# Optimization experiments

Hardware: AMD Instinct MI355X
Metric: run time of the kernel (lower is better)

## Reference

```python
import jax, jax.numpy as jnp
import numpy as np

EMBED_DIM = 1024
NUM_HEADS = 16
HEAD_DIM = EMBED_DIM // NUM_HEADS
SCALE = HEAD_DIM ** -0.5


def setup_inputs() -> dict:
    key = jax.random.key(0)
    ks = jax.random.split(key, 5)
    B, N, C = 4, 2048, EMBED_DIM
    s = C ** -0.5
    return {
        "x": jax.random.normal(ks[0], (B, N, C), dtype=jnp.float32),
        "w_qkv": jax.random.normal(ks[1], (C, 3 * C), dtype=jnp.float32) * s,
        "b_qkv": jnp.zeros((3 * C,), dtype=jnp.float32),
        "w_proj": jax.random.normal(ks[2], (C, C), dtype=jnp.float32) * s,
        "b_proj": jnp.zeros((C,), dtype=jnp.float32),
    }


def reference(x, w_qkv, b_qkv, w_proj, b_proj):
    B, N, C = x.shape
    H, D = NUM_HEADS, HEAD_DIM
    qkv = x @ w_qkv + b_qkv                      # (B, N, 3C)
    qkv = qkv.reshape(B, N, 3, H, D)
    qkv = jnp.transpose(qkv, (2, 0, 3, 1, 4))    # (3, B, H, N, D)
    q, k, v = qkv[0], qkv[1], qkv[2]
    attn = jnp.einsum('bhnd,bhmd->bhnm', q, k) * SCALE
    attn = jax.nn.softmax(attn, axis=-1)
    out = jnp.einsum('bhnm,bhmd->bhnd', attn, v)  # (B, H, N, D)
    out = jnp.transpose(out, (0, 2, 1, 3)).reshape(B, N, C)
    return out @ w_proj + b_proj
```

## Files before the change

kernel.cpp:

```cpp
#include <hip/hip_runtime.h>

typedef __attribute__((ext_vector_type(8))) short short8v;
typedef __attribute__((ext_vector_type(4))) short short4v;
typedef __attribute__((ext_vector_type(4))) float float4v;
typedef __attribute__((ext_vector_type(4))) unsigned short ushort4v;
typedef __attribute__((ext_vector_type(8))) unsigned short ushort8v;

#define GLOBAL_AS __attribute__((address_space(1)))
#define LDS_AS __attribute__((address_space(3)))

__device__ __forceinline__ void async_cp16(const void* g, void* l) {
  __builtin_amdgcn_global_load_lds((const GLOBAL_AS void*)g, (LDS_AS void*)l, 16, 0, 0);
}

__device__ __forceinline__ unsigned short f2bf(float f) {
  unsigned u = __float_as_uint(f);
  u += 0x7fffu + ((u >> 16) & 1u);
  return (unsigned short)(u >> 16);
}

#if defined(__HIP_DEVICE_COMPILE__)
#if __has_builtin(__builtin_amdgcn_mfma_f32_16x16x16bf16_1k)
#define MFMA_PV(a, b, c) __builtin_amdgcn_mfma_f32_16x16x16bf16_1k(a, b, c, 0, 0, 0)
#elif __has_builtin(__builtin_amdgcn_mfma_f32_16x16x16_bf16_1k)
#define MFMA_PV(a, b, c) __builtin_amdgcn_mfma_f32_16x16x16_bf16_1k(a, b, c, 0, 0, 0)
#elif __has_builtin(__builtin_amdgcn_mfma_f32_16x16x16_bf16)
#define MFMA_PV(a, b, c) __builtin_amdgcn_mfma_f32_16x16x16_bf16(a, b, c, 0, 0, 0)
#else
#error "no 16x16x16 bf16 mfma builtin on device"
#endif
#if __has_builtin(__builtin_amdgcn_exp2f)
#define EXP2F(x) __builtin_amdgcn_exp2f(x)
#else
#define EXP2F(x) exp2f(x)
#endif
#else
#define MFMA_PV(a, b, c) (c)
#define EXP2F(x) exp2f(x)
#endif

#if defined(__HIP_DEVICE_COMPILE__) && __has_builtin(__builtin_amdgcn_cvt_pk_bf16_f32)
typedef __attribute__((ext_vector_type(2))) __bf16 bf16x2v;
__device__ __forceinline__ unsigned pk_bf16(float a, float b) {
  bf16x2v r = __builtin_amdgcn_cvt_pk_bf16_f32(a, b);
  return __builtin_bit_cast(unsigned, r);
}
#else
__device__ __forceinline__ unsigned pk_bf16(float a, float b) {
  return (unsigned)f2bf(a) | ((unsigned)f2bf(b) << 16);
}
#endif

#define MFMA_QK(a, b, c) __builtin_amdgcn_mfma_f32_16x16x32_bf16(a, b, c, 0, 0, 0)


__global__ __launch_bounds__(256) void cvt_f32_bf16(const float* __restrict__ src,
                                                    unsigned short* __restrict__ dst) {
  int i = blockIdx.x * 256 + threadIdx.x;
  float4 v = ((const float4*)src)[i];
  ushort4v o;
  o.x = f2bf(v.x); o.y = f2bf(v.y); o.z = f2bf(v.z); o.w = f2bf(v.w);
  ((ushort4v*)dst)[i] = o;
}

__global__ __launch_bounds__(256) void transpose_w(const float* __restrict__ src,
                                                   unsigned short* __restrict__ dst,
                                                   int K, int N) {
  __shared__ float tile[64][65];
  int k0 = blockIdx.x * 64, n0 = blockIdx.y * 64;
  int t = threadIdx.x;
  int tc = t & 15, tr = t >> 4;
#pragma unroll
  for (int p = 0; p < 4; p++) {
    int r = tr + p * 16;
    float4 v = *(const float4*)(src + (size_t)(k0 + r) * N + n0 + tc * 4);
    tile[r][tc * 4 + 0] = v.x; tile[r][tc * 4 + 1] = v.y;
    tile[r][tc * 4 + 2] = v.z; tile[r][tc * 4 + 3] = v.w;
  }
  __syncthreads();
#pragma unroll
  for (int p = 0; p < 4; p++) {
    int rn = tr + p * 16;
    ushort4v o;
    o.x = f2bf(tile[tc * 4 + 0][rn]);
    o.y = f2bf(tile[tc * 4 + 1][rn]);
    o.z = f2bf(tile[tc * 4 + 2][rn]);
    o.w = f2bf(tile[tc * 4 + 3][rn]);
    *(ushort4v*)(dst + (size_t)(n0 + rn) * K + k0 + tc * 4) = o;
  }
}


__global__ __launch_bounds__(256) void gemm_qkv(const unsigned short* __restrict__ A,
                                                const unsigned short* __restrict__ BT,
                                                const float* __restrict__ bias,
                                                unsigned short* __restrict__ Qo,
                                                unsigned short* __restrict__ Ko,
                                                unsigned short* __restrict__ VTo) {
  __shared__ unsigned short As[128 * 32];
  __shared__ unsigned short Bs[128 * 32];
  int tid = threadIdx.x;
  int lane = tid & 63, w = tid >> 6, g = lane >> 4, c = lane & 15;
  int m0 = blockIdx.x * 128, n0 = blockIdx.y * 128;
  int wm = (w & 1) * 64, wn = (w >> 1) * 64;
  float4v acc[4][4] = {};

  for (int k0 = 0; k0 < 1024; k0 += 32) {
    __syncthreads();
#pragma unroll
    for (int p = 0; p < 2; p++) {
      int idx = p * 256 + tid;
      int row = idx >> 2, c8 = (idx & 3) * 8;
      async_cp16(A + (size_t)(m0 + row) * 1024 + k0 + c8, &As[idx * 8]);
      async_cp16(BT + (size_t)(n0 + row) * 1024 + k0 + c8, &Bs[idx * 8]);
    }
    __syncthreads();
    short8v af[4], bf[4];
#pragma unroll
    for (int i = 0; i < 4; i++)
      af[i] = *(const short8v*)(&As[(wm + i * 16 + c) * 32 + g * 8]);
#pragma unroll
    for (int j = 0; j < 4; j++)
      bf[j] = *(const short8v*)(&Bs[(wn + j * 16 + c) * 32 + g * 8]);
#pragma unroll
    for (int i = 0; i < 4; i++)
#pragma unroll
      for (int j = 0; j < 4; j++)
        acc[i][j] = MFMA_QK(af[i], bf[j], acc[i][j]);
  }

  int which = n0 >> 10;
#pragma unroll
  for (int j = 0; j < 4; j++) {
    int ng = n0 + wn + j * 16 + c;
    float bv = bias[ng];
    int h = (ng & 1023) >> 6, d = ng & 63;
#pragma unroll
    for (int i = 0; i < 4; i++) {
#pragma unroll
      for (int r = 0; r < 4; r++) {
        int mg = m0 + wm + i * 16 + g * 4 + r;
        int b = mg >> 11, n = mg & 2047;
        float v = acc[i][j][r] + bv;
        if (which == 0)
          Qo[((size_t)(b * 16 + h) * 2048 + n) * 64 + d] = f2bf(v * 0.18033688011112042f);
        else if (which == 1)
          Ko[((size_t)(b * 16 + h) * 2048 + n) * 64 + d] = f2bf(v);
        else
          VTo[((size_t)(b * 16 + h) * 64 + d) * 2048 + n] = f2bf(v);
      }
    }
  }
}


#define NTOK 2048
#define VTS 132

__global__ __launch_bounds__(256) void attn_kernel(const unsigned short* __restrict__ Qg,
                                                   const unsigned short* __restrict__ Kg,
                                                   const unsigned short* __restrict__ VTg,
                                                   unsigned short* __restrict__ Og) {
  __shared__ unsigned short Ks[128 * 64];
  __shared__ unsigned short VTsm[64 * VTS];

  int tid = threadIdx.x;
  int lane = tid & 63, w = tid >> 6, g = lane >> 4, c = lane & 15;
  int bh = blockIdx.y;
  int q0 = blockIdx.x * 128;

  const unsigned short* Qb = Qg + (size_t)bh * NTOK * 64;
  const unsigned short* Kb = Kg + (size_t)bh * NTOK * 64;
  const unsigned short* VTb = VTg + (size_t)bh * 64 * NTOK;

  short8v qf[2][2];
#pragma unroll
  for (int nt = 0; nt < 2; nt++)
#pragma unroll
    for (int kk = 0; kk < 2; kk++)
      qf[nt][kk] = *(const short8v*)(Qb + (size_t)(q0 + w * 32 + nt * 16 + c) * 64 +
                                     kk * 32 + g * 8);

  float4v L4[2] = {};
  float4v o[2][4] = {};

  for (int kt = 0; kt < NTOK; kt += 128) {
    __syncthreads();
#pragma unroll
    for (int p = 0; p < 4; p++) {
      int idx = p * 256 + tid;
      int row = idx >> 3, ch = idx & 7;
      async_cp16(Kb + (size_t)(kt + row) * 64 + ((ch ^ (row & 7)) * 8), &Ks[idx * 8]);
    }
    ushort8v vv[4];
    int vds[4], vcs[4];
#pragma unroll
    for (int p = 0; p < 4; p++) {
      int idx = p * 256 + tid;
      int d = idx >> 4, c8 = (idx & 15) * 8;
      vv[p] = *(const ushort8v*)(VTb + (size_t)d * NTOK + kt + c8);
      vds[p] = d; vcs[p] = c8;
    }
#pragma unroll
    for (int p = 0; p < 4; p++) {
      ushort4v lo = __builtin_shufflevector(vv[p], vv[p], 0, 1, 2, 3);
      ushort4v hi = __builtin_shufflevector(vv[p], vv[p], 4, 5, 6, 7);
      *(ushort4v*)(&VTsm[vds[p] * VTS + vcs[p]]) = lo;
      *(ushort4v*)(&VTsm[vds[p] * VTS + vcs[p] + 4]) = hi;
    }
    __syncthreads();

    float4v st[8][2] = {};
#pragma unroll
    for (int mt = 0; mt < 8; mt++) {
      int row = mt * 16 + c;
      short8v kf[2];
#pragma unroll
      for (int kk = 0; kk < 2; kk++) {
        int ch = (kk * 4 + g) ^ (row & 7);
        kf[kk] = *(const short8v*)(&Ks[row * 64 + ch * 8]);
      }
#pragma unroll
      for (int nt = 0; nt < 2; nt++)
#pragma unroll
        for (int kk = 0; kk < 2; kk++)
          st[mt][nt] = MFMA_QK(kf[kk], qf[nt][kk], st[mt][nt]);
    }

#pragma unroll
    for (int nt = 0; nt < 2; nt++)
#pragma unroll
      for (int mt = 0; mt < 8; mt++) {
        float4v s4 = st[mt][nt];
        s4.x = EXP2F(s4.x); s4.y = EXP2F(s4.y);
        s4.z = EXP2F(s4.z); s4.w = EXP2F(s4.w);
        st[mt][nt] = s4;
        L4[nt] += s4;
      }

#pragma unroll
    for (int kk8 = 0; kk8 < 8; kk8++) {
      short4v pa[2];
#pragma unroll
      for (int nt = 0; nt < 2; nt++) {
        float4v p4 = st[kk8][nt];
        union { unsigned u[2]; short4v s; } cv;
        cv.u[0] = pk_bf16(p4.x, p4.y);
        cv.u[1] = pk_bf16(p4.z, p4.w);
        pa[nt] = cv.s;
      }
#pragma unroll
      for (int nt_o = 0; nt_o < 4; nt_o++) {
        short4v vb = *(const short4v*)(&VTsm[(nt_o * 16 + c) * VTS + kk8 * 16 + g * 4]);
#pragma unroll
        for (int mt_o = 0; mt_o < 2; mt_o++)
          o[mt_o][nt_o] = MFMA_PV(pa[mt_o], vb, o[mt_o][nt_o]);
      }
    }
  }

  float L[2];
#pragma unroll
  for (int nt = 0; nt < 2; nt++) {
    float l = L4[nt].x + L4[nt].y + L4[nt].z + L4[nt].w;
    l += __shfl_xor(l, 16);
    l += __shfl_xor(l, 32);
    L[nt] = l;
  }
  int b = bh >> 4, h = bh & 15;
#pragma unroll
  for (int mt_o = 0; mt_o < 2; mt_o++) {
    float4v li;
#pragma unroll
    for (int r = 0; r < 4; r++) li[r] = 1.0f / __shfl(L[mt_o], g * 4 + r);
#pragma unroll
    for (int nt_o = 0; nt_o < 4; nt_o++) {
      float4v v = o[mt_o][nt_o] * li;
      int col = h * 64 + nt_o * 16 + c;
      int rowbase = b * NTOK + q0 + w * 32 + mt_o * 16 + g * 4;
#pragma unroll
      for (int r = 0; r < 4; r++)
        Og[(size_t)(rowbase + r) * 1024 + col] = f2bf(v[r]);
    }
  }
}

__global__ __launch_bounds__(256) void gemm_proj(const unsigned short* __restrict__ A,
                                                 const unsigned short* __restrict__ BT,
                                                 const float* __restrict__ bias,
                                                 float* __restrict__ out) {
  __shared__ unsigned short As[128 * 32];
  __shared__ unsigned short Bs[128 * 32];
  int tid = threadIdx.x;
  int lane = tid & 63, w = tid >> 6, g = lane >> 4, c = lane & 15;
  int m0 = blockIdx.x * 128, n0 = blockIdx.y * 128;
  int wm = (w & 1) * 64, wn = (w >> 1) * 64;
  float4v acc[4][4] = {};

  for (int k0 = 0; k0 < 1024; k0 += 32) {
    __syncthreads();
#pragma unroll
    for (int p = 0; p < 2; p++) {
      int idx = p * 256 + tid;
      int row = idx >> 2, c8 = (idx & 3) * 8;
      async_cp16(A + (size_t)(m0 + row) * 1024 + k0 + c8, &As[idx * 8]);
      async_cp16(BT + (size_t)(n0 + row) * 1024 + k0 + c8, &Bs[idx * 8]);
    }
    __syncthreads();
    short8v af[4], bf[4];
#pragma unroll
    for (int i = 0; i < 4; i++)
      af[i] = *(const short8v*)(&As[(wm + i * 16 + c) * 32 + g * 8]);
#pragma unroll
    for (int j = 0; j < 4; j++)
      bf[j] = *(const short8v*)(&Bs[(wn + j * 16 + c) * 32 + g * 8]);
#pragma unroll
    for (int i = 0; i < 4; i++)
#pragma unroll
      for (int j = 0; j < 4; j++)
        acc[i][j] = MFMA_QK(af[i], bf[j], acc[i][j]);
  }

#pragma unroll
  for (int j = 0; j < 4; j++) {
    int ng = n0 + wn + j * 16 + c;
    float bv = bias[ng];
#pragma unroll
    for (int i = 0; i < 4; i++) {
#pragma unroll
      for (int r = 0; r < 4; r++) {
        int mg = m0 + wm + i * 16 + g * 4 + r;
        out[(size_t)mg * 1024 + ng] = acc[i][j][r] + bv;
      }
    }
  }
}


extern "C" void kernel_launch(void* const* d_in, const int* in_sizes, int n_in,
                              void* d_out, int out_size, void* d_ws, size_t ws_size,
                              hipStream_t stream) {
  (void)in_sizes; (void)n_in; (void)out_size; (void)ws_size;
  const float* x = (const float*)d_in[0];
  const float* w_qkv = (const float*)d_in[1];
  const float* b_qkv = (const float*)d_in[2];
  const float* w_proj = (const float*)d_in[3];
  const float* b_proj = (const float*)d_in[4];
  float* out = (float*)d_out;

  unsigned short* x_bf = (unsigned short*)d_ws;
  unsigned short* wqkvT = x_bf + (size_t)8192 * 1024;
  unsigned short* wprojT = wqkvT + (size_t)3072 * 1024;
  unsigned short* qws = wprojT + (size_t)1024 * 1024;
  unsigned short* kws = qws + (size_t)8388608;
  unsigned short* vtws = kws + (size_t)8388608;
  unsigned short* aws = vtws + (size_t)8388608;

  cvt_f32_bf16<<<8192, 256, 0, stream>>>(x, x_bf);
  transpose_w<<<dim3(16, 48), 256, 0, stream>>>(w_qkv, wqkvT, 1024, 3072);
  transpose_w<<<dim3(16, 16), 256, 0, stream>>>(w_proj, wprojT, 1024, 1024);
  gemm_qkv<<<dim3(64, 24), 256, 0, stream>>>(x_bf, wqkvT, b_qkv, qws, kws, vtws);
  attn_kernel<<<dim3(16, 64), 256, 0, stream>>>(qws, kws, vtws, aws);
  gemm_proj<<<dim3(64, 8), 256, 0, stream>>>(aws, wprojT, b_proj, out);
}
```

Before: 303.6 us.

## Split attention tile into halves and compute softmax row sums via MFMA with ones

```diff
diff --git a/kernel.cpp b/kernel.cpp
--- a/kernel.cpp
+++ b/kernel.cpp
@@ -181,7 +181,11 @@
       qf[nt][kk] = *(const short8v*)(Qb + (size_t)(q0 + w * 32 + nt * 16 + c) * 64 +
                                      kk * 32 + g * 8);
 
-  float4v L4[2] = {};
+  short4v ones;
+  ones.x = (short)0x3F80; ones.y = (short)0x3F80;
+  ones.z = (short)0x3F80; ones.w = (short)0x3F80;
+
+  float4v lacc[2] = {};
   float4v o[2][4] = {};
 
   for (int kt = 0; kt < NTOK; kt += 128) {
@@ -210,69 +214,60 @@
     }
     __syncthreads();
 
-    float4v st[8][2] = {};
-#pragma unroll
-    for (int mt = 0; mt < 8; mt++) {
-      int row = mt * 16 + c;
-      short8v kf[2];
-#pragma unroll
-      for (int kk = 0; kk < 2; kk++) {
-        int ch = (kk * 4 + g) ^ (row & 7);
-        kf[kk] = *(const short8v*)(&Ks[row * 64 + ch * 8]);
+#pragma unroll
+    for (int half = 0; half < 2; half++) {
+      float4v st[4][2] = {};
+#pragma unroll
+      for (int mth = 0; mth < 4; mth++) {
+        int mt = half * 4 + mth;
+        int row = mt * 16 + c;
+        short8v kf[2];
+#pragma unroll
+        for (int kk = 0; kk < 2; kk++) {
+          int ch = (kk * 4 + g) ^ (row & 7);
+          kf[kk] = *(const short8v*)(&Ks[row * 64 + ch * 8]);
+        }
+#pragma unroll
+        for (int nt = 0; nt < 2; nt++)
+#pragma unroll
+          for (int kk = 0; kk < 2; kk++)
+            st[mth][nt] = MFMA_QK(kf[kk], qf[nt][kk], st[mth][nt]);
       }
-#pragma unroll
-      for (int nt = 0; nt < 2; nt++)
-#pragma unroll
-        for (int kk = 0; kk < 2; kk++)
-          st[mt][nt] = MFMA_QK(kf[kk], qf[nt][kk], st[mt][nt]);
-    }
-
-#pragma unroll
-    for (int nt = 0; nt < 2; nt++)
-#pragma unroll
-      for (int mt = 0; mt < 8; mt++) {
-        float4v s4 = st[mt][nt];
-        s4.x = EXP2F(s4.x); s4.y = EXP2F(s4.y);
-        s4.z = EXP2F(s4.z); s4.w = EXP2F(s4.w);
-        st[mt][nt] = s4;
-        L4[nt] += s4;
+
+#pragma unroll
+      for (int mth = 0; mth < 4; mth++) {
+        int kk8 = half * 4 + mth;
+        short4v pa[2];
+#pragma unroll
+        for (int nt = 0; nt < 2; nt++) {
+          float4v p4 = st[mth][nt];
+          p4.x = EXP2F(p4.x); p4.y = EXP2F(p4.y);
+          p4.z = EXP2F(p4.z); p4.w = EXP2F(p4.w);
+          union { unsigned u[2]; short4v s; } cv;
+          cv.u[0] = pk_bf16(p4.x, p4.y);
+          cv.u[1] = pk_bf16(p4.z, p4.w);
+          pa[nt] = cv.s;
+        }
+#pragma unroll
+        for (int nt_o = 0; nt_o < 4; nt_o++) {
+          short4v vb = *(const short4v*)(&VTsm[(nt_o * 16 + c) * VTS + kk8 * 16 + g * 4]);
+#pragma unroll
+          for (int mt_o = 0; mt_o < 2; mt_o++)
+            o[mt_o][nt_o] = MFMA_PV(pa[mt_o], vb, o[mt_o][nt_o]);
+        }
+#pragma unroll
+        for (int mt_o = 0; mt_o < 2; mt_o++)
+          lacc[mt_o] = MFMA_PV(pa[mt_o], ones, lacc[mt_o]);
       }
-
-#pragma unroll
-    for (int kk8 = 0; kk8 < 8; kk8++) {
-      short4v pa[2];
-#pragma unroll
-      for (int nt = 0; nt < 2; nt++) {
-        float4v p4 = st[kk8][nt];
-        union { unsigned u[2]; short4v s; } cv;
-        cv.u[0] = pk_bf16(p4.x, p4.y);
-        cv.u[1] = pk_bf16(p4.z, p4.w);
-        pa[nt] = cv.s;
-      }
-#pragma unroll
-      for (int nt_o = 0; nt_o < 4; nt_o++) {
-        short4v vb = *(const short4v*)(&VTsm[(nt_o * 16 + c) * VTS + kk8 * 16 + g * 4]);
-#pragma unroll
-        for (int mt_o = 0; mt_o < 2; mt_o++)
-          o[mt_o][nt_o] = MFMA_PV(pa[mt_o], vb, o[mt_o][nt_o]);
-      }
-    }
-  }
-
-  float L[2];
-#pragma unroll
-  for (int nt = 0; nt < 2; nt++) {
-    float l = L4[nt].x + L4[nt].y + L4[nt].z + L4[nt].w;
-    l += __shfl_xor(l, 16);
-    l += __shfl_xor(l, 32);
-    L[nt] = l;
-  }
+    }
+  }
+
   int b = bh >> 4, h = bh & 15;
 #pragma unroll
   for (int mt_o = 0; mt_o < 2; mt_o++) {
     float4v li;
 #pragma unroll
-    for (int r = 0; r < 4; r++) li[r] = 1.0f / __shfl(L[mt_o], g * 4 + r);
+    for (int r = 0; r < 4; r++) li[r] = 1.0f / lacc[mt_o][r];
 #pragma unroll
     for (int nt_o = 0; nt_o < 4; nt_o++) {
       float4v v = o[mt_o][nt_o] * li;
```

After: 312.1 us. +2.8%, slower.
